# Kernel optimization log

Measured on AMD Instinct MI355X. Metric: run time of the kernel, lower is better.

## Reference

```python
import jax, jax.numpy as jnp
import numpy as np

D_MODEL = 1024
D_FF = 4 * D_MODEL
NUM_TILES = 8
B, T = 4, 2048


def setup_inputs() -> dict:
    key = jax.random.key(0)
    ks = jax.random.split(key, 7)
    s = 0.02
    return {
        "x": jax.random.normal(ks[0], (B, T, D_MODEL), dtype=jnp.float32),
        "gate_W": jax.random.normal(ks[1], (D_MODEL, NUM_TILES), dtype=jnp.float32) * s,
        "gate_b": jnp.zeros((NUM_TILES,), dtype=jnp.float32),
        "up_W": jax.random.normal(ks[2], (NUM_TILES, D_MODEL, D_FF), dtype=jnp.float32) * s,
        "up_b": jnp.zeros((NUM_TILES, D_FF), dtype=jnp.float32),
        "down_W": jax.random.normal(ks[3], (NUM_TILES, D_FF, D_MODEL), dtype=jnp.float32) * s,
        "down_b": jnp.zeros((NUM_TILES, D_MODEL), dtype=jnp.float32),
    }


def top1_gate(logits):
    # Hard one-hot of argmax; straight-through identity gradient (Top1Gate).
    hard = jax.nn.one_hot(jnp.argmax(logits, axis=-1), logits.shape[-1], dtype=logits.dtype)
    return hard + (logits - jax.lax.stop_gradient(logits))


def trix_linear(x, gate, W, b):
    # x: [N, I], gate: [N, E] one-hot, W: [E, I, O], b: [E, O]
    # Per-tile linear combined by gate weight; loop over small fixed E.
    out = jnp.zeros((x.shape[0], W.shape[2]), dtype=x.dtype)
    for e in range(W.shape[0]):
        out = out + gate[:, e:e + 1] * (x @ W[e] + b[e])
    return out


def reference(x, gate_W, gate_b, up_W, up_b, down_W, down_b):
    Bv, Tv, C = x.shape
    xf = x.reshape(Bv * Tv, C)                      # [N, C]
    gate = top1_gate(xf @ gate_W + gate_b)          # [N, E]
    h = jax.nn.relu(trix_linear(xf, gate, up_W, up_b))   # [N, 4C]
    # dropout in eval mode (identity)
    out = trix_linear(h, gate, down_W, down_b)      # [N, C]
    return out.reshape(Bv, Tv, C), gate.reshape(Bv, Tv, -1)
```

## Files before the change

### kernel.cpp

```cpp
#include <hip/hip_runtime.h>
#include <hip/hip_bf16.h>
#include <stdint.h>

#define NTOK 8192
#define DM   1024
#define DFF  4096
#define NE   8

typedef __bf16 bf16x8 __attribute__((ext_vector_type(8)));
typedef short  short8 __attribute__((ext_vector_type(8)));
typedef float  floatx4 __attribute__((ext_vector_type(4)));

#define WS_CNT   0
#define WS_OFF   64
#define WS_EIDX  1024
#define WS_PERM  (WS_EIDX + NTOK * 4)
#define WS_XPERM (WS_PERM + NTOK * 4)
#define WS_HPERM (WS_XPERM + (NTOK + 128) * DM * 2)

__device__ __forceinline__ unsigned short f2bf(float f) {
  union { float f; unsigned u; } v; v.f = f;
  return (unsigned short)((v.u + 0x7FFFu + ((v.u >> 16) & 1u)) >> 16);
}

__device__ __forceinline__ float f4get(const float4& v, int i) {
  return i == 0 ? v.x : i == 1 ? v.y : i == 2 ? v.z : v.w;
}

__global__ __launch_bounds__(256) void gate_kernel(
    const float* __restrict__ x, const float* __restrict__ gW,
    const float* __restrict__ gb, float* __restrict__ gate_out,
    int* __restrict__ eidx) {
  int wave = threadIdx.x >> 6;
  int lane = threadIdx.x & 63;
  int t = blockIdx.x * 4 + wave;
  const float4* xr = (const float4*)(x + (size_t)t * DM + lane * 16);
  float acc[8] = {0, 0, 0, 0, 0, 0, 0, 0};
#pragma unroll
  for (int q = 0; q < 4; ++q) {
    float4 xv = xr[q];
    int kbase = lane * 16 + q * 4;
#pragma unroll
    for (int d = 0; d < 4; ++d) {
      float xs = f4get(xv, d);
      const float4* g4 = (const float4*)(gW + (size_t)(kbase + d) * NE);
      float4 g0 = g4[0], g1 = g4[1];
      acc[0] += xs * g0.x; acc[1] += xs * g0.y;
      acc[2] += xs * g0.z; acc[3] += xs * g0.w;
      acc[4] += xs * g1.x; acc[5] += xs * g1.y;
      acc[6] += xs * g1.z; acc[7] += xs * g1.w;
    }
  }
#pragma unroll
  for (int off = 32; off > 0; off >>= 1) {
#pragma unroll
    for (int e = 0; e < 8; ++e) acc[e] += __shfl_down(acc[e], off);
  }
  if (lane == 0) {
    float best = acc[0] + gb[0];
    int bi = 0;
#pragma unroll
    for (int e = 1; e < 8; ++e) {
      float v = acc[e] + gb[e];
      if (v > best) { best = v; bi = e; }
    }
#pragma unroll
    for (int e = 0; e < 8; ++e) gate_out[(size_t)t * NE + e] = (e == bi) ? 1.0f : 0.0f;
    eidx[t] = bi;
  }
}

__global__ __launch_bounds__(1024) void rank_kernel(
    const int* __restrict__ eidx, int* __restrict__ counts,
    int* __restrict__ offs, int* __restrict__ perm) {
  __shared__ unsigned long long sa[1024], sb[1024];
  int tid = threadIdx.x;
  int e8[8];
  unsigned long long ca = 0, cb = 0;
#pragma unroll
  for (int j = 0; j < 8; ++j) {
    int e = eidx[tid * 8 + j];
    e8[j] = e;
    if (e < 4) ca += 1ull << (16 * e);
    else       cb += 1ull << (16 * (e - 4));
  }
  sa[tid] = ca; sb[tid] = cb;
  __syncthreads();
  for (int off = 1; off < 1024; off <<= 1) {
    unsigned long long ta = 0, tb = 0;
    if (tid >= off) { ta = sa[tid - off]; tb = sb[tid - off]; }
    __syncthreads();
    sa[tid] += ta; sb[tid] += tb;
    __syncthreads();
  }
  unsigned long long tot_a = sa[1023], tot_b = sb[1023];
  int cnt_e[8];
#pragma unroll
  for (int e = 0; e < 4; ++e) cnt_e[e] = (int)((tot_a >> (16 * e)) & 0xFFFF);
#pragma unroll
  for (int e = 0; e < 4; ++e) cnt_e[e + 4] = (int)((tot_b >> (16 * e)) & 0xFFFF);
  int off_e[8]; int s = 0;
#pragma unroll
  for (int e = 0; e < 8; ++e) { off_e[e] = s; s += cnt_e[e]; }
  if (tid < 8) { counts[tid] = cnt_e[tid]; offs[tid] = off_e[tid]; }
  unsigned long long ia = sa[tid] - ca, ib = sb[tid] - cb;
  int run[8];
#pragma unroll
  for (int e = 0; e < 4; ++e) run[e] = (int)((ia >> (16 * e)) & 0xFFFF);
#pragma unroll
  for (int e = 0; e < 4; ++e) run[e + 4] = (int)((ib >> (16 * e)) & 0xFFFF);
#pragma unroll
  for (int j = 0; j < 8; ++j) {
    int e = e8[j];
    int pos = off_e[e] + run[e]++;
    perm[pos] = tid * 8 + j;
  }
}

__global__ __launch_bounds__(256) void scatter_data_kernel(
    const float* __restrict__ x, const int* __restrict__ perm,
    unsigned short* __restrict__ xperm) {
  int wave = threadIdx.x >> 6, lane = threadIdx.x & 63;
  int p = blockIdx.x * 4 + wave;
  int t = perm[p];
  const float4* xr = (const float4*)(x + (size_t)t * DM);
#pragma unroll
  for (int q = 0; q < 4; ++q) {
    float4 v = xr[q * 64 + lane];
    uint2 pk;
    pk.x = (unsigned)f2bf(v.x) | ((unsigned)f2bf(v.y) << 16);
    pk.y = (unsigned)f2bf(v.z) | ((unsigned)f2bf(v.w) << 16);
    *(uint2*)(xperm + (size_t)p * DM + q * 256 + lane * 4) = pk;
  }
}

__global__ __launch_bounds__(256) void up_gemm_kernel(
    const unsigned short* __restrict__ xperm,
    const float* __restrict__ upW, const float* __restrict__ upB,
    const int* __restrict__ counts, const int* __restrict__ offs,
    unsigned short* __restrict__ hperm) {
  int e = blockIdx.y >> 6;
  int mt = blockIdx.y & 63;
  int cnt = counts[e];
  if (mt * 128 >= cnt) return;
  int row0 = offs[e] + mt * 128;
  int rows_valid = cnt - mt * 128; if (rows_valid > 128) rows_valid = 128;
  int n0 = blockIdx.x * 128;
  const float* Bg = upW + (size_t)e * DM * DFF;

  __shared__ unsigned short sA[128 * 40];
  __shared__ unsigned short sB[128 * 40];

  int tid = threadIdx.x;
  int wave = tid >> 6, lane = tid & 63;
  int wm = (wave >> 1) * 64, wn = (wave & 1) * 64;

  floatx4 acc[4][4];
#pragma unroll
  for (int i = 0; i < 4; ++i)
#pragma unroll
    for (int j = 0; j < 4; ++j) acc[i][j] = (floatx4){0.f, 0.f, 0.f, 0.f};

  int ar = tid >> 2;
  int ac = (tid & 3) * 8;
  int nq = (tid & 31) * 4;
  int kq = (tid >> 5) * 4;

  for (int k0 = 0; k0 < DM; k0 += 32) {
    __syncthreads();
#pragma unroll
    for (int p = 0; p < 2; ++p) {
      int r = p * 64 + ar;
      short8 av = *(const short8*)(xperm + (size_t)(row0 + r) * DM + k0 + ac);
      *(short8*)(sA + r * 40 + ac) = av;
    }
    float4 bv[4];
#pragma unroll
    for (int dk = 0; dk < 4; ++dk)
      bv[dk] = *(const float4*)(Bg + (size_t)(k0 + kq + dk) * DFF + n0 + nq);
#pragma unroll
    for (int dn = 0; dn < 4; ++dn) {
      uint2 pk;
      pk.x = (unsigned)f2bf(f4get(bv[0], dn)) | ((unsigned)f2bf(f4get(bv[1], dn)) << 16);
      pk.y = (unsigned)f2bf(f4get(bv[2], dn)) | ((unsigned)f2bf(f4get(bv[3], dn)) << 16);
      *(uint2*)(sB + (nq + dn) * 40 + kq) = pk;
    }
    __syncthreads();
    bf16x8 a[4], b[4];
#pragma unroll
    for (int i = 0; i < 4; ++i)
      a[i] = *(const bf16x8*)(sA + (wm + i * 16 + (lane & 15)) * 40 + (lane >> 4) * 8);
#pragma unroll
    for (int j = 0; j < 4; ++j)
      b[j] = *(const bf16x8*)(sB + (wn + j * 16 + (lane & 15)) * 40 + (lane >> 4) * 8);
#pragma unroll
    for (int i = 0; i < 4; ++i)
#pragma unroll
      for (int j = 0; j < 4; ++j)
        acc[i][j] = __builtin_amdgcn_mfma_f32_16x16x32_bf16(a[i], b[j], acc[i][j], 0, 0, 0);
  }

  const float* ub = upB + (size_t)e * DFF;
#pragma unroll
  for (int i = 0; i < 4; ++i) {
#pragma unroll
    for (int r = 0; r < 4; ++r) {
      int rl = wm + i * 16 + (lane >> 4) * 4 + r;
      if (rl < rows_valid) {
        size_t rowg = (size_t)(row0 + rl) * DFF;
#pragma unroll
        for (int j = 0; j < 4; ++j) {
          int col = n0 + wn + j * 16 + (lane & 15);
          float v = acc[i][j][r] + ub[col];
          v = v > 0.f ? v : 0.f;
          hperm[rowg + col] = f2bf(v);
        }
      }
    }
  }
}

__global__ __launch_bounds__(256) void down_gemm_kernel(
    const unsigned short* __restrict__ hperm,
    const float* __restrict__ dW, const float* __restrict__ dB,
    const int* __restrict__ counts, const int* __restrict__ offs,
    const int* __restrict__ perm, float* __restrict__ out) {
  int e = blockIdx.y >> 6;
  int mt = blockIdx.y & 63;
  int cnt = counts[e];
  if (mt * 128 >= cnt) return;
  int row0 = offs[e] + mt * 128;
  int rows_valid = cnt - mt * 128; if (rows_valid > 128) rows_valid = 128;
  int n0 = blockIdx.x * 128;
  const float* Bg = dW + (size_t)e * DFF * DM;

  __shared__ unsigned short sA[128 * 40];
  __shared__ unsigned short sB[128 * 40];

  int tid = threadIdx.x;
  int wave = tid >> 6, lane = tid & 63;
  int wm = (wave >> 1) * 64, wn = (wave & 1) * 64;

  floatx4 acc[4][4];
#pragma unroll
  for (int i = 0; i < 4; ++i)
#pragma unroll
    for (int j = 0; j < 4; ++j) acc[i][j] = (floatx4){0.f, 0.f, 0.f, 0.f};

  int ar = tid >> 2;
  int ac = (tid & 3) * 8;
  int nq = (tid & 31) * 4;
  int kq = (tid >> 5) * 4;

  for (int k0 = 0; k0 < DFF; k0 += 32) {
    __syncthreads();
#pragma unroll
    for (int p = 0; p < 2; ++p) {
      int r = p * 64 + ar;
      short8 av = *(const short8*)(hperm + (size_t)(row0 + r) * DFF + k0 + ac);
      *(short8*)(sA + r * 40 + ac) = av;
    }
    float4 bv[4];
#pragma unroll
    for (int dk = 0; dk < 4; ++dk)
      bv[dk] = *(const float4*)(Bg + (size_t)(k0 + kq + dk) * DM + n0 + nq);
#pragma unroll
    for (int dn = 0; dn < 4; ++dn) {
      uint2 pk;
      pk.x = (unsigned)f2bf(f4get(bv[0], dn)) | ((unsigned)f2bf(f4get(bv[1], dn)) << 16);
      pk.y = (unsigned)f2bf(f4get(bv[2], dn)) | ((unsigned)f2bf(f4get(bv[3], dn)) << 16);
      *(uint2*)(sB + (nq + dn) * 40 + kq) = pk;
    }
    __syncthreads();
    bf16x8 a[4], b[4];
#pragma unroll
    for (int i = 0; i < 4; ++i)
      a[i] = *(const bf16x8*)(sA + (wm + i * 16 + (lane & 15)) * 40 + (lane >> 4) * 8);
#pragma unroll
    for (int j = 0; j < 4; ++j)
      b[j] = *(const bf16x8*)(sB + (wn + j * 16 + (lane & 15)) * 40 + (lane >> 4) * 8);
#pragma unroll
    for (int i = 0; i < 4; ++i)
#pragma unroll
      for (int j = 0; j < 4; ++j)
        acc[i][j] = __builtin_amdgcn_mfma_f32_16x16x32_bf16(a[i], b[j], acc[i][j], 0, 0, 0);
  }

  const float* db = dB + (size_t)e * DM;
#pragma unroll
  for (int i = 0; i < 4; ++i) {
#pragma unroll
    for (int r = 0; r < 4; ++r) {
      int rl = wm + i * 16 + (lane >> 4) * 4 + r;
      if (rl < rows_valid) {
        int token = perm[row0 + rl];
        size_t og = (size_t)token * DM;
#pragma unroll
        for (int j = 0; j < 4; ++j) {
          int col = n0 + wn + j * 16 + (lane & 15);
          out[og + col] = acc[i][j][r] + db[col];
        }
      }
    }
  }
}

extern "C" void kernel_launch(void* const* d_in, const int* in_sizes, int n_in,
                              void* d_out, int out_size, void* d_ws, size_t ws_size,
                              hipStream_t stream) {
  const float* x   = (const float*)d_in[0];
  const float* gW  = (const float*)d_in[1];
  const float* gb  = (const float*)d_in[2];
  const float* upW = (const float*)d_in[3];
  const float* upB = (const float*)d_in[4];
  const float* dW  = (const float*)d_in[5];
  const float* dB  = (const float*)d_in[6];
  float* out      = (float*)d_out;
  float* gate_out = out + (size_t)NTOK * DM;

  char* ws = (char*)d_ws;
  int* cnt  = (int*)(ws + WS_CNT);
  int* off  = (int*)(ws + WS_OFF);
  int* eidx = (int*)(ws + WS_EIDX);
  int* perm = (int*)(ws + WS_PERM);
  unsigned short* xperm = (unsigned short*)(ws + WS_XPERM);
  unsigned short* hperm = (unsigned short*)(ws + WS_HPERM);

  gate_kernel<<<NTOK / 4, 256, 0, stream>>>(x, gW, gb, gate_out, eidx);
  rank_kernel<<<1, 1024, 0, stream>>>(eidx, cnt, off, perm);
  scatter_data_kernel<<<NTOK / 4, 256, 0, stream>>>(x, perm, xperm);
  up_gemm_kernel<<<dim3(DFF / 128, NE * 64), 256, 0, stream>>>(xperm, upW, upB, cnt, off, hperm);
  down_gemm_kernel<<<dim3(DM / 128, NE * 64), 256, 0, stream>>>(hperm, dW, dB, cnt, off, perm, out);
}
```

Baseline: 668.9 us.

## Pre-transpose weights to bf16 and use direct-to-LDS loads with split-K down GEMM

Adds a pass that converts each expert's fp32 weights into a transposed bf16 copy in workspace, so the GEMM inner loops can stream both operands with global_load_lds instead of converting fp32 weights on every tile. A compact tile list built in the rank kernel replaces the sparse 512-row grid with 72 rows, removing most early-exit blocks. The down GEMM splits K in two and accumulates with float atomics into an output pre-filled with the bias. The trade-offs are an extra full weight read and write per call, a larger workspace requirement with fallback to the old path, no double buffering, and nondeterministic atomic summation.

```diff
diff --git a/kernel.cpp b/kernel.cpp
--- a/kernel.cpp
+++ b/kernel.cpp
@@ -13,10 +13,17 @@
 
 #define WS_CNT   0
 #define WS_OFF   64
+#define WS_TINFO 128
 #define WS_EIDX  1024
 #define WS_PERM  (WS_EIDX + NTOK * 4)
 #define WS_XPERM (WS_PERM + NTOK * 4)
-#define WS_HPERM (WS_XPERM + (NTOK + 128) * DM * 2)
+#define XPERM_BYTES ((size_t)(NTOK + 128) * DM * 2)
+#define WS_WT    (WS_XPERM + XPERM_BYTES)
+#define WT_BYTES ((size_t)NE * DM * DFF * 2)
+#define WS_HPERM_FAST (WS_WT + WT_BYTES)
+#define HPERM_BYTES ((size_t)(NTOK + 128) * DFF * 2)
+#define FAST_NEED (WS_HPERM_FAST + HPERM_BYTES)
+#define WS_HPERM_FB (WS_XPERM + XPERM_BYTES)
 
 __device__ __forceinline__ unsigned short f2bf(float f) {
   union { float f; unsigned u; } v; v.f = f;
@@ -25,6 +32,12 @@
 
 __device__ __forceinline__ float f4get(const float4& v, int i) {
   return i == 0 ? v.x : i == 1 ? v.y : i == 2 ? v.z : v.w;
+}
+
+__device__ __forceinline__ void gl16(const void* g, void* l) {
+  __builtin_amdgcn_global_load_lds(
+      (const __attribute__((address_space(1))) unsigned int*)g,
+      (__attribute__((address_space(3))) unsigned int*)l, 16, 0, 0);
 }
 
 __global__ __launch_bounds__(256) void gate_kernel(
@@ -72,7 +85,7 @@
 
 __global__ __launch_bounds__(1024) void rank_kernel(
     const int* __restrict__ eidx, int* __restrict__ counts,
-    int* __restrict__ offs, int* __restrict__ perm) {
+    int* __restrict__ offs, int* __restrict__ tinfo, int* __restrict__ perm) {
   __shared__ unsigned long long sa[1024], sb[1024];
   int tid = threadIdx.x;
   int e8[8];
@@ -103,6 +116,14 @@
 #pragma unroll
   for (int e = 0; e < 8; ++e) { off_e[e] = s; s += cnt_e[e]; }
   if (tid < 8) { counts[tid] = cnt_e[tid]; offs[tid] = off_e[tid]; }
+  if (tid == 0) {
+    int nt = 0;
+    for (int e = 0; e < 8; ++e) {
+      int ntile = (cnt_e[e] + 127) >> 7;
+      for (int m = 0; m < ntile; ++m) tinfo[1 + nt++] = (e << 16) | m;
+    }
+    tinfo[0] = nt;
+  }
   unsigned long long ia = sa[tid] - ca, ib = sb[tid] - cb;
   int run[8];
 #pragma unroll
@@ -131,6 +152,203 @@
     pk.x = (unsigned)f2bf(v.x) | ((unsigned)f2bf(v.y) << 16);
     pk.y = (unsigned)f2bf(v.z) | ((unsigned)f2bf(v.w) << 16);
     *(uint2*)(xperm + (size_t)p * DM + q * 256 + lane * 4) = pk;
+  }
+}
+
+__global__ __launch_bounds__(256) void wtrans_kernel(
+    const float* __restrict__ W, unsigned short* __restrict__ Wt, int K, int N) {
+  __shared__ uint2 sT[64 * 17];
+  int e = blockIdx.z;
+  const float* We = W + (size_t)e * K * N;
+  unsigned short* Wte = Wt + (size_t)e * K * N;
+  int n0 = blockIdx.x * 64, k0 = blockIdx.y * 64;
+  int t = threadIdx.x;
+  int kg = t >> 4;
+  int ng = t & 15;
+  float4 r[4];
+#pragma unroll
+  for (int j = 0; j < 4; ++j)
+    r[j] = *(const float4*)(We + (size_t)(k0 + kg * 4 + j) * N + n0 + ng * 4);
+#pragma unroll
+  for (int i = 0; i < 4; ++i) {
+    uint2 pk;
+    pk.x = (unsigned)f2bf(f4get(r[0], i)) | ((unsigned)f2bf(f4get(r[1], i)) << 16);
+    pk.y = (unsigned)f2bf(f4get(r[2], i)) | ((unsigned)f2bf(f4get(r[3], i)) << 16);
+    sT[(ng * 4 + i) * 17 + kg] = pk;
+  }
+  __syncthreads();
+  int n = t >> 2, q = t & 3;
+  uint2 a = sT[n * 17 + q * 4 + 0], b = sT[n * 17 + q * 4 + 1];
+  uint2 c = sT[n * 17 + q * 4 + 2], d = sT[n * 17 + q * 4 + 3];
+  uint4 w0 = make_uint4(a.x, a.y, b.x, b.y);
+  uint4 w1 = make_uint4(c.x, c.y, d.x, d.y);
+  uint4* dst = (uint4*)(Wte + (size_t)(n0 + n) * K + k0 + q * 16);
+  dst[0] = w0; dst[1] = w1;
+}
+
+__global__ __launch_bounds__(256) void init_out_kernel(
+    const int* __restrict__ eidx, const float* __restrict__ dB,
+    float* __restrict__ out) {
+  int wave = threadIdx.x >> 6, lane = threadIdx.x & 63;
+  int t = blockIdx.x * 4 + wave;
+  int e = eidx[t];
+  const float4* src = (const float4*)(dB + (size_t)e * DM);
+  float4* dst = (float4*)(out + (size_t)t * DM);
+#pragma unroll
+  for (int q = 0; q < 4; ++q) dst[q * 64 + lane] = src[q * 64 + lane];
+}
+
+__global__ __launch_bounds__(256) void up_gemm2(
+    const unsigned short* __restrict__ xperm,
+    const unsigned short* __restrict__ upWt,
+    const float* __restrict__ upB,
+    const int* __restrict__ tinfo, const int* __restrict__ offs,
+    const int* __restrict__ counts, unsigned short* __restrict__ hperm) {
+  if ((int)blockIdx.y >= tinfo[0]) return;
+  int pk = tinfo[1 + blockIdx.y];
+  int e = pk >> 16, mt = pk & 0xFFFF;
+  int cnt = counts[e];
+  int row0 = offs[e] + mt * 128;
+  int rows_valid = cnt - mt * 128; if (rows_valid > 128) rows_valid = 128;
+  int n0 = blockIdx.x * 128;
+  const unsigned short* Bg = upWt + (size_t)e * DFF * DM + (size_t)n0 * DM;
+
+  __shared__ __align__(16) unsigned short sA[128 * 32];
+  __shared__ __align__(16) unsigned short sB[128 * 32];
+
+  int tid = threadIdx.x, w = tid >> 6, lane = tid & 63;
+  int wm = (w >> 1) * 64, wn = (w & 1) * 64;
+
+  int sr = w * 16 + (lane >> 2);
+  int sseg = (lane & 3) * 8;
+  const unsigned short* ga0 = xperm + (size_t)(row0 + sr) * DM + sseg;
+  const unsigned short* ga1 = xperm + (size_t)(row0 + 64 + sr) * DM + sseg;
+  const unsigned short* gb0 = Bg + (size_t)sr * DM + sseg;
+  const unsigned short* gb1 = Bg + (size_t)(64 + sr) * DM + sseg;
+  unsigned short* la0 = sA + w * 512;
+  unsigned short* la1 = sA + 2048 + w * 512;
+  unsigned short* lb0 = sB + w * 512;
+  unsigned short* lb1 = sB + 2048 + w * 512;
+
+  floatx4 acc[4][4];
+#pragma unroll
+  for (int i = 0; i < 4; ++i)
+#pragma unroll
+    for (int j = 0; j < 4; ++j) acc[i][j] = (floatx4){0.f, 0.f, 0.f, 0.f};
+
+  for (int k0 = 0; k0 < DM; k0 += 32) {
+    __syncthreads();
+    gl16(ga0 + k0, la0); gl16(ga1 + k0, la1);
+    gl16(gb0 + k0, lb0); gl16(gb1 + k0, lb1);
+    __syncthreads();
+    bf16x8 a[4], b[4];
+#pragma unroll
+    for (int i = 0; i < 4; ++i)
+      a[i] = *(const bf16x8*)(sA + (wm + i * 16 + (lane & 15)) * 32 + (lane >> 4) * 8);
+#pragma unroll
+    for (int j = 0; j < 4; ++j)
+      b[j] = *(const bf16x8*)(sB + (wn + j * 16 + (lane & 15)) * 32 + (lane >> 4) * 8);
+#pragma unroll
+    for (int i = 0; i < 4; ++i)
+#pragma unroll
+      for (int j = 0; j < 4; ++j)
+        acc[i][j] = __builtin_amdgcn_mfma_f32_16x16x32_bf16(a[i], b[j], acc[i][j], 0, 0, 0);
+  }
+
+  const float* ub = upB + (size_t)e * DFF;
+#pragma unroll
+  for (int i = 0; i < 4; ++i) {
+#pragma unroll
+    for (int r = 0; r < 4; ++r) {
+      int rl = wm + i * 16 + (lane >> 4) * 4 + r;
+      if (rl < rows_valid) {
+        size_t rowg = (size_t)(row0 + rl) * DFF;
+#pragma unroll
+        for (int j = 0; j < 4; ++j) {
+          int col = n0 + wn + j * 16 + (lane & 15);
+          float v = acc[i][j][r] + ub[col];
+          v = v > 0.f ? v : 0.f;
+          hperm[rowg + col] = f2bf(v);
+        }
+      }
+    }
+  }
+}
+
+__global__ __launch_bounds__(256) void down_gemm2(
+    const unsigned short* __restrict__ hperm,
+    const unsigned short* __restrict__ dWt,
+    const int* __restrict__ tinfo, const int* __restrict__ offs,
+    const int* __restrict__ counts, const int* __restrict__ perm,
+    float* __restrict__ out) {
+  if ((int)blockIdx.y >= tinfo[0]) return;
+  int pk = tinfo[1 + blockIdx.y];
+  int e = pk >> 16, mt = pk & 0xFFFF;
+  int cnt = counts[e];
+  int row0 = offs[e] + mt * 128;
+  int rows_valid = cnt - mt * 128; if (rows_valid > 128) rows_valid = 128;
+  int n0 = blockIdx.x * 128;
+  int kz = blockIdx.z;
+  const unsigned short* Bg = dWt + (size_t)e * DM * DFF + (size_t)n0 * DFF;
+
+  __shared__ __align__(16) unsigned short sA[128 * 32];
+  __shared__ __align__(16) unsigned short sB[128 * 32];
+
+  int tid = threadIdx.x, w = tid >> 6, lane = tid & 63;
+  int wm = (w >> 1) * 64, wn = (w & 1) * 64;
+
+  int sr = w * 16 + (lane >> 2);
+  int sseg = (lane & 3) * 8;
+  const unsigned short* ga0 = hperm + (size_t)(row0 + sr) * DFF + sseg;
+  const unsigned short* ga1 = hperm + (size_t)(row0 + 64 + sr) * DFF + sseg;
+  const unsigned short* gb0 = Bg + (size_t)sr * DFF + sseg;
+  const unsigned short* gb1 = Bg + (size_t)(64 + sr) * DFF + sseg;
+  unsigned short* la0 = sA + w * 512;
+  unsigned short* la1 = sA + 2048 + w * 512;
+  unsigned short* lb0 = sB + w * 512;
+  unsigned short* lb1 = sB + 2048 + w * 512;
+
+  floatx4 acc[4][4];
+#pragma unroll
+  for (int i = 0; i < 4; ++i)
+#pragma unroll
+    for (int j = 0; j < 4; ++j) acc[i][j] = (floatx4){0.f, 0.f, 0.f, 0.f};
+
+  int kbeg = kz * (DFF / 2), kend = kbeg + DFF / 2;
+  for (int k0 = kbeg; k0 < kend; k0 += 32) {
+    __syncthreads();
+    gl16(ga0 + k0, la0); gl16(ga1 + k0, la1);
+    gl16(gb0 + k0, lb0); gl16(gb1 + k0, lb1);
+    __syncthreads();
+    bf16x8 a[4], b[4];
+#pragma unroll
+    for (int i = 0; i < 4; ++i)
+      a[i] = *(const bf16x8*)(sA + (wm + i * 16 + (lane & 15)) * 32 + (lane >> 4) * 8);
+#pragma unroll
+    for (int j = 0; j < 4; ++j)
+      b[j] = *(const bf16x8*)(sB + (wn + j * 16 + (lane & 15)) * 32 + (lane >> 4) * 8);
+#pragma unroll
+    for (int i = 0; i < 4; ++i)
+#pragma unroll
+      for (int j = 0; j < 4; ++j)
+        acc[i][j] = __builtin_amdgcn_mfma_f32_16x16x32_bf16(a[i], b[j], acc[i][j], 0, 0, 0);
+  }
+
+#pragma unroll
+  for (int i = 0; i < 4; ++i) {
+#pragma unroll
+    for (int r = 0; r < 4; ++r) {
+      int rl = wm + i * 16 + (lane >> 4) * 4 + r;
+      if (rl < rows_valid) {
+        int token = perm[row0 + rl];
+        size_t og = (size_t)token * DM;
+#pragma unroll
+        for (int j = 0; j < 4; ++j) {
+          int col = n0 + wn + j * 16 + (lane & 15);
+          atomicAdd(&out[og + col], acc[i][j][r]);
+        }
+      }
+    }
   }
 }
 
@@ -147,25 +365,17 @@
   int rows_valid = cnt - mt * 128; if (rows_valid > 128) rows_valid = 128;
   int n0 = blockIdx.x * 128;
   const float* Bg = upW + (size_t)e * DM * DFF;
-
   __shared__ unsigned short sA[128 * 40];
   __shared__ unsigned short sB[128 * 40];
-
   int tid = threadIdx.x;
   int wave = tid >> 6, lane = tid & 63;
   int wm = (wave >> 1) * 64, wn = (wave & 1) * 64;
-
   floatx4 acc[4][4];
 #pragma unroll
   for (int i = 0; i < 4; ++i)
 #pragma unroll
     for (int j = 0; j < 4; ++j) acc[i][j] = (floatx4){0.f, 0.f, 0.f, 0.f};
-
-  int ar = tid >> 2;
-  int ac = (tid & 3) * 8;
-  int nq = (tid & 31) * 4;
-  int kq = (tid >> 5) * 4;
-
+  int ar = tid >> 2, ac = (tid & 3) * 8, nq = (tid & 31) * 4, kq = (tid >> 5) * 4;
   for (int k0 = 0; k0 < DM; k0 += 32) {
     __syncthreads();
 #pragma unroll
@@ -199,7 +409,6 @@
       for (int j = 0; j < 4; ++j)
         acc[i][j] = __builtin_amdgcn_mfma_f32_16x16x32_bf16(a[i], b[j], acc[i][j], 0, 0, 0);
   }
-
   const float* ub = upB + (size_t)e * DFF;
 #pragma unroll
   for (int i = 0; i < 4; ++i) {
@@ -233,25 +442,17 @@
   int rows_valid = cnt - mt * 128; if (rows_valid > 128) rows_valid = 128;
   int n0 = blockIdx.x * 128;
   const float* Bg = dW + (size_t)e * DFF * DM;
-
   __shared__ unsigned short sA[128 * 40];
   __shared__ unsigned short sB[128 * 40];
-
   int tid = threadIdx.x;
   int wave = tid >> 6, lane = tid & 63;
   int wm = (wave >> 1) * 64, wn = (wave & 1) * 64;
-
   floatx4 acc[4][4];
 #pragma unroll
   for (int i = 0; i < 4; ++i)
 #pragma unroll
     for (int j = 0; j < 4; ++j) acc[i][j] = (floatx4){0.f, 0.f, 0.f, 0.f};
-
-  int ar = tid >> 2;
-  int ac = (tid & 3) * 8;
-  int nq = (tid & 31) * 4;
-  int kq = (tid >> 5) * 4;
-
+  int ar = tid >> 2, ac = (tid & 3) * 8, nq = (tid & 31) * 4, kq = (tid >> 5) * 4;
   for (int k0 = 0; k0 < DFF; k0 += 32) {
     __syncthreads();
 #pragma unroll
@@ -285,7 +486,6 @@
       for (int j = 0; j < 4; ++j)
         acc[i][j] = __builtin_amdgcn_mfma_f32_16x16x32_bf16(a[i], b[j], acc[i][j], 0, 0, 0);
   }
-
   const float* db = dB + (size_t)e * DM;
 #pragma unroll
   for (int i = 0; i < 4; ++i) {
@@ -319,16 +519,28 @@
   float* gate_out = out + (size_t)NTOK * DM;
 
   char* ws = (char*)d_ws;
-  int* cnt  = (int*)(ws + WS_CNT);
-  int* off  = (int*)(ws + WS_OFF);
-  int* eidx = (int*)(ws + WS_EIDX);
-  int* perm = (int*)(ws + WS_PERM);
+  int* cnt   = (int*)(ws + WS_CNT);
+  int* off   = (int*)(ws + WS_OFF);
+  int* tinfo = (int*)(ws + WS_TINFO);
+  int* eidx  = (int*)(ws + WS_EIDX);
+  int* perm  = (int*)(ws + WS_PERM);
   unsigned short* xperm = (unsigned short*)(ws + WS_XPERM);
-  unsigned short* hperm = (unsigned short*)(ws + WS_HPERM);
 
   gate_kernel<<<NTOK / 4, 256, 0, stream>>>(x, gW, gb, gate_out, eidx);
-  rank_kernel<<<1, 1024, 0, stream>>>(eidx, cnt, off, perm);
+  rank_kernel<<<1, 1024, 0, stream>>>(eidx, cnt, off, tinfo, perm);
   scatter_data_kernel<<<NTOK / 4, 256, 0, stream>>>(x, perm, xperm);
-  up_gemm_kernel<<<dim3(DFF / 128, NE * 64), 256, 0, stream>>>(xperm, upW, upB, cnt, off, hperm);
-  down_gemm_kernel<<<dim3(DM / 128, NE * 64), 256, 0, stream>>>(hperm, dW, dB, cnt, off, perm, out);
-}
+
+  if (ws_size >= FAST_NEED) {
+    unsigned short* wt    = (unsigned short*)(ws + WS_WT);
+    unsigned short* hperm = (unsigned short*)(ws + WS_HPERM_FAST);
+    wtrans_kernel<<<dim3(DFF / 64, DM / 64, NE), 256, 0, stream>>>(upW, wt, DM, DFF);
+    up_gemm2<<<dim3(DFF / 128, 72), 256, 0, stream>>>(xperm, wt, upB, tinfo, off, cnt, hperm);
+    wtrans_kernel<<<dim3(DM / 64, DFF / 64, NE), 256, 0, stream>>>(dW, wt, DFF, DM);
+    init_out_kernel<<<NTOK / 4, 256, 0, stream>>>(eidx, dB, out);
+    down_gemm2<<<dim3(DM / 128, 72, 2), 256, 0, stream>>>(hperm, wt, tinfo, off, cnt, perm, out);
+  } else {
+    unsigned short* hperm = (unsigned short*)(ws + WS_HPERM_FB);
+    up_gemm_kernel<<<dim3(DFF / 128, NE * 64), 256, 0, stream>>>(xperm, upW, upB, cnt, off, hperm);
+    down_gemm_kernel<<<dim3(DM / 128, NE * 64), 256, 0, stream>>>(hperm, dW, dB, cnt, off, perm, out);
+  }
+}
```

Result: no change. 672.0 us (+0.5%).
